# Optimization experiments

Hardware: AMD Instinct MI355X
Metric: run time of the kernel (lower is better)

Reference implementation:

```python
import jax, jax.numpy as jnp
import numpy as np

B, N, M = 8, 256, 256
C_IN, C_MID, C_OUT = 64, 256, 256


def setup_inputs() -> dict:
    key = jax.random.key(0)
    k1, k2, k3, k4 = jax.random.split(key, 4)
    x = jax.random.normal(k1, (B, N, M, C_IN), dtype=jnp.float32)
    # nn.Linear(in_channels, mid_channels): weight (mid, in), bias (mid)
    w1 = jax.random.normal(k2, (C_MID, C_IN), dtype=jnp.float32) * (1.0 / np.sqrt(C_IN))
    b1 = jax.random.normal(k3, (C_MID,), dtype=jnp.float32) * 0.01
    # nn.Linear(in+mid, out, bias=False): weight (out, in+mid)
    w2 = jax.random.normal(k4, (C_OUT, C_IN + C_MID), dtype=jnp.float32) * (1.0 / np.sqrt(C_IN + C_MID))
    return {"x": x, "w1": w1, "b1": b1, "w2": w2, "dim_target": 2}


def reference(x, w1, b1, w2, dim_target):
    # first_process: Linear over last dim -> (B, N, M, C_MID)
    z = jnp.einsum('bnmc,dc->bnmd', x, w1) + b1
    # MaxPoolingAggregator: max over dim_target keepdim, then expand back over M
    z_vertex = jnp.max(z, axis=dim_target, keepdims=True)  # (B, N, 1, C_MID)
    z_vertex = jnp.broadcast_to(z_vertex, z.shape)          # (B, N, M, C_MID)
    # ConcatMerger(dim_feature=-1): cat edge features x with vertex features
    merged = jnp.concatenate([x, z_vertex], axis=-1)        # (B, N, M, C_IN+C_MID)
    # second_process: bias-free Linear -> (B, N, M, C_OUT)
    return jnp.einsum('bnmc,dc->bnmd', merged, w2)
```

## Files before the change

kernel.cpp:

```cpp
#include <hip/hip_runtime.h>


#define CIN  64
#define KPAD 72
#define PLANE 18432

typedef __attribute__((ext_vector_type(8))) short short8;
typedef __attribute__((ext_vector_type(4))) float float4v;

__device__ __forceinline__ short f2bf(float f) {
    union { float f; unsigned u; } c; c.f = f;
    unsigned u = c.u;
    unsigned r = (u + 0x7FFFu + ((u >> 16) & 1u)) >> 16;
    return (short)r;
}
__device__ __forceinline__ float bf2f(short s) {
    union { unsigned u; float f; } c;
    c.u = ((unsigned)(unsigned short)s) << 16;
    return c.f;
}

__global__ void prep_weights(const float* __restrict__ w1,
                             const float* __restrict__ w2,
                             short* __restrict__ wsS) {
    int i = blockIdx.x * 256 + threadIdx.x;
    if (i < 16384) {
        float f = w1[i];
        short h = f2bf(f);
        wsS[i] = h;
        wsS[16384 + i] = f2bf(f - bf2f(h));
    } else if (i < 32768) {
        int q = i - 16384;
        int j = q >> 6, k = q & 63;
        float f = w2[j * 320 + k];
        short h = f2bf(f);
        wsS[32768 + q] = h;
        wsS[49152 + q] = f2bf(f - bf2f(h));
    } else if (i < 98304) {
        int q = i - 32768;
        int d = q >> 8, j = q & 255;
        ((float*)(wsS + 65536))[q] = w2[j * 320 + 64 + d];
    }
}

__global__ __launch_bounds__(256, 2)
void fused_pointnet(const float* __restrict__ x,
                    const float* __restrict__ b1,
                    const short* __restrict__ w1p,
                    const short* __restrict__ w2xp,
                    const float* __restrict__ w2zt,
                    float* __restrict__ out) {
    __shared__ short wlds[2 * PLANE];
    __shared__ float red[1024];
    __shared__ float zv[256];
    __shared__ float vv[256];

    const int tid = threadIdx.x;
    const int bn  = blockIdx.x;
    const int w   = tid >> 6;
    const int l   = tid & 63;
    const int dl  = l & 15;
    const int q   = l >> 4;
    const int mw  = w * 64;
    const float* __restrict__ xg = x + (size_t)bn * (256 * CIN);

    float4 xa0[4][2], xa1[4][2];
#pragma unroll
    for (int t = 0; t < 4; ++t)
#pragma unroll
        for (int s = 0; s < 2; ++s) {
            const float* p = xg + (mw + t * 16 + dl) * CIN + s * 32 + q * 8;
            xa0[t][s] = *(const float4*)p;
            xa1[t][s] = *(const float4*)(p + 4);
        }

    {
        const short8* src = (const short8*)w1p;
#pragma unroll
        for (int it = 0; it < 16; ++it) {
            int i = tid + 256 * it;
            int plane = i >> 11;
            int c = i & 2047;
            int row = c >> 3, k = (c & 7) << 3;
            *(short8*)&wlds[plane * PLANE + row * KPAD + k] = src[i];
        }
    }

    short8 ahi[4][2], alo[4][2];
#pragma unroll
    for (int t = 0; t < 4; ++t)
#pragma unroll
        for (int s = 0; s < 2; ++s) {
            float e[8];
            e[0] = xa0[t][s].x; e[1] = xa0[t][s].y; e[2] = xa0[t][s].z; e[3] = xa0[t][s].w;
            e[4] = xa1[t][s].x; e[5] = xa1[t][s].y; e[6] = xa1[t][s].z; e[7] = xa1[t][s].w;
#pragma unroll
            for (int j = 0; j < 8; ++j) {
                short h = f2bf(e[j]);
                ahi[t][s][j] = h;
                alo[t][s][j] = f2bf(e[j] - bf2f(h));
            }
        }
    __syncthreads();

#pragma unroll
    for (int chunk = 0; chunk < 4; ++chunk) {
        const int d0c = chunk * 64;
        short8 bhi[4][2], blo[4][2];
#pragma unroll
        for (int dt = 0; dt < 4; ++dt)
#pragma unroll
            for (int s = 0; s < 2; ++s) {
                int off = (d0c + dt * 16 + dl) * KPAD + s * 32 + q * 8;
                bhi[dt][s] = *(const short8*)&wlds[off];
                blo[dt][s] = *(const short8*)&wlds[off + PLANE];
            }
        float4v acc[4][4];
#pragma unroll
        for (int t = 0; t < 4; ++t)
#pragma unroll
            for (int dt = 0; dt < 4; ++dt) {
                float4v a = {0.f, 0.f, 0.f, 0.f};
#pragma unroll
                for (int s = 0; s < 2; ++s) {
                    a = __builtin_amdgcn_mfma_f32_16x16x32_bf16(ahi[t][s], bhi[dt][s], a, 0, 0, 0);
                    a = __builtin_amdgcn_mfma_f32_16x16x32_bf16(ahi[t][s], blo[dt][s], a, 0, 0, 0);
                    a = __builtin_amdgcn_mfma_f32_16x16x32_bf16(alo[t][s], bhi[dt][s], a, 0, 0, 0);
                }
                acc[t][dt] = a;
            }
#pragma unroll
        for (int dt = 0; dt < 4; ++dt) {
            float mx = -3.0e38f;
#pragma unroll
            for (int t = 0; t < 4; ++t)
#pragma unroll
                for (int r = 0; r < 4; ++r) mx = fmaxf(mx, acc[t][dt][r]);
            mx = fmaxf(mx, __shfl_xor(mx, 16));
            mx = fmaxf(mx, __shfl_xor(mx, 32));
            if (q == 0) red[w * 256 + d0c + dt * 16 + dl] = mx;
        }
    }
    __syncthreads();
    zv[tid] = fmaxf(fmaxf(red[tid], red[256 + tid]),
                    fmaxf(red[512 + tid], red[768 + tid])) + b1[tid];
    __syncthreads();

    {
        const short8* src = (const short8*)w2xp;
#pragma unroll
        for (int it = 0; it < 16; ++it) {
            int i = tid + 256 * it;
            int plane = i >> 11;
            int c = i & 2047;
            int row = c >> 3, k = (c & 7) << 3;
            *(short8*)&wlds[plane * PLANE + row * KPAD + k] = src[i];
        }
    }
    {
        const int jq = tid & 63;
        const int dpart = tid >> 6;
        const float4* wz4 = (const float4*)w2zt;
        float4 vacc = make_float4(0.f, 0.f, 0.f, 0.f);
#pragma unroll 4
        for (int d = 0; d < 64; ++d) {
            int dd = dpart * 64 + d;
            float s = zv[dd];
            float4 wv = wz4[dd * 64 + jq];
            vacc.x = fmaf(s, wv.x, vacc.x);
            vacc.y = fmaf(s, wv.y, vacc.y);
            vacc.z = fmaf(s, wv.z, vacc.z);
            vacc.w = fmaf(s, wv.w, vacc.w);
        }
        ((float4*)red)[dpart * 64 + jq] = vacc;
    }
    __syncthreads();
    vv[tid] = red[tid] + red[256 + tid] + red[512 + tid] + red[768 + tid];
    __syncthreads();

    float* __restrict__ og = out + (size_t)bn * (256 * 256);
#pragma unroll
    for (int chunk = 0; chunk < 4; ++chunk) {
        const int d0c = chunk * 64;
        short8 bhi[4][2], blo[4][2];
#pragma unroll
        for (int dt = 0; dt < 4; ++dt)
#pragma unroll
            for (int s = 0; s < 2; ++s) {
                int off = (d0c + dt * 16 + dl) * KPAD + s * 32 + q * 8;
                bhi[dt][s] = *(const short8*)&wlds[off];
                blo[dt][s] = *(const short8*)&wlds[off + PLANE];
            }
        float vdt[4];
#pragma unroll
        for (int dt = 0; dt < 4; ++dt) vdt[dt] = vv[d0c + dt * 16 + dl];
#pragma unroll
        for (int t = 0; t < 4; ++t)
#pragma unroll
            for (int dt = 0; dt < 4; ++dt) {
                float4v a = {0.f, 0.f, 0.f, 0.f};
#pragma unroll
                for (int s = 0; s < 2; ++s) {
                    a = __builtin_amdgcn_mfma_f32_16x16x32_bf16(ahi[t][s], bhi[dt][s], a, 0, 0, 0);
                    a = __builtin_amdgcn_mfma_f32_16x16x32_bf16(ahi[t][s], blo[dt][s], a, 0, 0, 0);
                    a = __builtin_amdgcn_mfma_f32_16x16x32_bf16(alo[t][s], bhi[dt][s], a, 0, 0, 0);
                }
                const int rowb = (mw + t * 16 + q * 4) * 256 + d0c + dt * 16 + dl;
#pragma unroll
                for (int r = 0; r < 4; ++r)
                    og[rowb + r * 256] = a[r] + vdt[dt];
            }
    }
}

extern "C" void kernel_launch(void* const* d_in, const int* in_sizes, int n_in,
                              void* d_out, int out_size, void* d_ws, size_t ws_size,
                              hipStream_t stream) {
    const float* x  = (const float*)d_in[0];
    const float* w1 = (const float*)d_in[1];
    const float* b1 = (const float*)d_in[2];
    const float* w2 = (const float*)d_in[3];
    short* wsS = (short*)d_ws;
    float* out = (float*)d_out;

    hipLaunchKernelGGL(prep_weights, dim3(384), dim3(256), 0, stream, w1, w2, wsS);
    hipLaunchKernelGGL(fused_pointnet, dim3(2048), dim3(256), 0, stream,
                       x, b1, wsS, wsS + 32768, (const float*)(wsS + 65536), out);
}
```

Measured before the change: 639.9 us.

## Split fused kernel into vertex-vector and output kernels with nontemporal stores

Splits the single fused kernel into two. The first computes the per-(b,n) max-pooled vertex projection and writes it to a workspace buffer. The second reloads x, applies the second GEMM, and writes the output with nontemporal stores. This is meant to cut per-kernel register and LDS pressure and to let the output-heavy phase run with its own schedule. The cost is reading x twice from global memory and an extra launch.

```diff
diff --git a/kernel.cpp b/kernel.cpp
--- a/kernel.cpp
+++ b/kernel.cpp
@@ -44,16 +44,14 @@
 }
 
 __global__ __launch_bounds__(256, 2)
-void fused_pointnet(const float* __restrict__ x,
-                    const float* __restrict__ b1,
-                    const short* __restrict__ w1p,
-                    const short* __restrict__ w2xp,
-                    const float* __restrict__ w2zt,
-                    float* __restrict__ out) {
+void compute_vv(const float* __restrict__ x,
+                const float* __restrict__ b1,
+                const short* __restrict__ w1p,
+                const float* __restrict__ w2zt,
+                float* __restrict__ vvg) {
     __shared__ short wlds[2 * PLANE];
     __shared__ float red[1024];
     __shared__ float zv[256];
-    __shared__ float vv[256];
 
     const int tid = threadIdx.x;
     const int bn  = blockIdx.x;
@@ -146,17 +144,6 @@
                     fmaxf(red[512 + tid], red[768 + tid])) + b1[tid];
     __syncthreads();
 
-    {
-        const short8* src = (const short8*)w2xp;
-#pragma unroll
-        for (int it = 0; it < 16; ++it) {
-            int i = tid + 256 * it;
-            int plane = i >> 11;
-            int c = i & 2047;
-            int row = c >> 3, k = (c & 7) << 3;
-            *(short8*)&wlds[plane * PLANE + row * KPAD + k] = src[i];
-        }
-    }
     {
         const int jq = tid & 63;
         const int dpart = tid >> 6;
@@ -175,7 +162,64 @@
         ((float4*)red)[dpart * 64 + jq] = vacc;
     }
     __syncthreads();
-    vv[tid] = red[tid] + red[256 + tid] + red[512 + tid] + red[768 + tid];
+    vvg[bn * 256 + tid] = red[tid] + red[256 + tid] + red[512 + tid] + red[768 + tid];
+}
+
+__global__ __launch_bounds__(256, 2)
+void apply_out(const float* __restrict__ x,
+               const short* __restrict__ w2xp,
+               const float* __restrict__ vvg,
+               float* __restrict__ out) {
+    __shared__ short wlds[2 * PLANE];
+    __shared__ float vvs[256];
+
+    const int tid = threadIdx.x;
+    const int bn  = blockIdx.x;
+    const int w   = tid >> 6;
+    const int l   = tid & 63;
+    const int dl  = l & 15;
+    const int q   = l >> 4;
+    const int mw  = w * 64;
+    const float* __restrict__ xg = x + (size_t)bn * (256 * CIN);
+
+    float4 xa0[4][2], xa1[4][2];
+#pragma unroll
+    for (int t = 0; t < 4; ++t)
+#pragma unroll
+        for (int s = 0; s < 2; ++s) {
+            const float* p = xg + (mw + t * 16 + dl) * CIN + s * 32 + q * 8;
+            xa0[t][s] = *(const float4*)p;
+            xa1[t][s] = *(const float4*)(p + 4);
+        }
+
+    {
+        const short8* src = (const short8*)w2xp;
+#pragma unroll
+        for (int it = 0; it < 16; ++it) {
+            int i = tid + 256 * it;
+            int plane = i >> 11;
+            int c = i & 2047;
+            int row = c >> 3, k = (c & 7) << 3;
+            *(short8*)&wlds[plane * PLANE + row * KPAD + k] = src[i];
+        }
+    }
+    vvs[tid] = vvg[bn * 256 + tid];
+
+    short8 ahi[4][2], alo[4][2];
+#pragma unroll
+    for (int t = 0; t < 4; ++t)
+#pragma unroll
+        for (int s = 0; s < 2; ++s) {
+            float e[8];
+            e[0] = xa0[t][s].x; e[1] = xa0[t][s].y; e[2] = xa0[t][s].z; e[3] = xa0[t][s].w;
+            e[4] = xa1[t][s].x; e[5] = xa1[t][s].y; e[6] = xa1[t][s].z; e[7] = xa1[t][s].w;
+#pragma unroll
+            for (int j = 0; j < 8; ++j) {
+                short h = f2bf(e[j]);
+                ahi[t][s][j] = h;
+                alo[t][s][j] = f2bf(e[j] - bf2f(h));
+            }
+        }
     __syncthreads();
 
     float* __restrict__ og = out + (size_t)bn * (256 * 256);
@@ -193,7 +237,7 @@
             }
         float vdt[4];
 #pragma unroll
-        for (int dt = 0; dt < 4; ++dt) vdt[dt] = vv[d0c + dt * 16 + dl];
+        for (int dt = 0; dt < 4; ++dt) vdt[dt] = vvs[d0c + dt * 16 + dl];
 #pragma unroll
         for (int t = 0; t < 4; ++t)
 #pragma unroll
@@ -208,7 +252,7 @@
                 const int rowb = (mw + t * 16 + q * 4) * 256 + d0c + dt * 16 + dl;
 #pragma unroll
                 for (int r = 0; r < 4; ++r)
-                    og[rowb + r * 256] = a[r] + vdt[dt];
+                    __builtin_nontemporal_store(a[r] + vdt[dt], &og[rowb + r * 256]);
             }
     }
 }
@@ -222,8 +266,11 @@
     const float* w2 = (const float*)d_in[3];
     short* wsS = (short*)d_ws;
     float* out = (float*)d_out;
+    float* vvg = (float*)(wsS + 196608);
 
     hipLaunchKernelGGL(prep_weights, dim3(384), dim3(256), 0, stream, w1, w2, wsS);
-    hipLaunchKernelGGL(fused_pointnet, dim3(2048), dim3(256), 0, stream,
-                       x, b1, wsS, wsS + 32768, (const float*)(wsS + 65536), out);
-}
+    hipLaunchKernelGGL(compute_vv, dim3(2048), dim3(256), 0, stream,
+                       x, b1, wsS, (const float*)(wsS + 65536), vvg);
+    hipLaunchKernelGGL(apply_out, dim3(2048), dim3(256), 0, stream,
+                       x, wsS + 32768, vvg, out);
+}
```

After: 718.3 us. 12.2% more time.
